# Performance work log

Hardware: AMD Instinct MI355X
Metric: run time of the kernel (lower is better)

Reference implementation:

```python
import jax, jax.numpy as jnp
import numpy as np

B, S, D_IN, D_OUT = 4, 2048, 1024, 1024

def setup_inputs() -> dict:
    key = jax.random.key(0)
    k1, k2, k3, k4 = jax.random.split(key, 4)
    s = 0.02
    return {
        "X": jax.random.normal(k1, (B, S, D_IN), dtype=jnp.float32),
        "Wq": jax.random.normal(k2, (D_OUT, D_IN), dtype=jnp.float32) * s,
        "Wk": jax.random.normal(k3, (D_OUT, D_IN), dtype=jnp.float32) * s,
        "Wv": jax.random.normal(k4, (D_OUT, D_IN), dtype=jnp.float32) * s,
    }

def reference(X, Wq, Wk, Wv):
    # nn.Linear: y = x @ W.T (no bias)
    q = jnp.einsum('bsd,ed->bse', X, Wq)  # [B,S,D_OUT]
    k = jnp.einsum('bsd,ed->bse', X, Wk)
    v = jnp.einsum('bsd,ed->bse', X, Wv)
    scores = jnp.einsum('bqe,bke->bqk', q, k)  # [B,S,S]
    n = X.shape[1]
    causal = jnp.triu(jnp.ones((n, n), dtype=bool), k=1)
    scores = jnp.where(causal[None], -jnp.inf, scores)
    scale = 1.0 / jnp.sqrt(jnp.asarray(k.shape[-1], dtype=scores.dtype))
    attn = jax.nn.softmax(scores * scale, axis=-1)
    return jnp.einsum('bqk,bke->bqe', attn, v)
```

## Files before the change

kernel.cpp:

```cpp
#include <hip/hip_runtime.h>
#include <cstdint>


typedef __attribute__((ext_vector_type(8))) __bf16 bf16x8;
typedef __attribute__((ext_vector_type(4))) float f32x4;

#define BK 64

__device__ __forceinline__ unsigned short f2bf(float f) {
  union { float f; unsigned u; } v; v.f = f;
  unsigned r = v.u + 0x7fffu + ((v.u >> 16) & 1u);
  return (unsigned short)(r >> 16);
}

__device__ __forceinline__ void gload_lds16(const void* g, void* l) {
  __builtin_amdgcn_global_load_lds(
      (const __attribute__((address_space(1))) void*)g,
      (__attribute__((address_space(3))) void*)l, 16, 0, 0);
}

__global__ __launch_bounds__(256)
void cvt_all(const float* __restrict__ X, const float* __restrict__ Wq,
             const float* __restrict__ Wk, const float* __restrict__ Wv,
             unsigned short* __restrict__ Xbf, unsigned short* __restrict__ Wall,
             float* __restrict__ L) {
  const int bid = blockIdx.x;
  if (bid >= 11264) {
    float4* p = (float4*)(L + (size_t)(bid - 11264) * 2048);
    p[threadIdx.x] = (float4){0.f, 0.f, 0.f, 0.f};
    p[threadIdx.x + 256] = (float4){0.f, 0.f, 0.f, 0.f};
    return;
  }
  const float* src;
  unsigned short* dst;
  int i;
  if (bid < 8192) {
    src = X; dst = Xbf; i = bid * 256 + threadIdx.x;
  } else {
    const int m = bid - 8192;
    const int sel = m >> 10;
    src = (sel == 0) ? Wq : (sel == 1) ? Wk : Wv;
    dst = Wall + (size_t)sel * 1048576;
    i = (m & 1023) * 256 + threadIdx.x;
  }
  float4 v = ((const float4*)src)[i];
  ushort4 o;
  o.x = f2bf(v.x); o.y = f2bf(v.y); o.z = f2bf(v.z); o.w = f2bf(v.w);
  ((ushort4*)dst)[i] = o;
}

__global__ __launch_bounds__(256, 3)
void gemm_qkv(const unsigned short* __restrict__ A,
              const unsigned short* __restrict__ Bm,
              unsigned short* __restrict__ Qb,
              unsigned short* __restrict__ Kb,
              unsigned short* __restrict__ Vt)
{
  const int bx = blockIdx.x, by = blockIdx.y;

  __shared__ __align__(16) unsigned short As[128 * BK];
  __shared__ __align__(16) unsigned short Bs[128 * BK];

  const int tid = threadIdx.x;
  const int wave = tid >> 6, lane = tid & 63;
  const int wr = wave >> 1, wc = wave & 1;
  const int quad = lane >> 4, l16 = lane & 15;

  const unsigned rsub = wave * 8 + (lane >> 3);
  const unsigned csb = (unsigned)(((lane & 7) ^ ((lane >> 3) & 7)) * 16);

  unsigned offA[4], offB[4];
  #pragma unroll
  for (int s = 0; s < 4; ++s) {
    offA[s] = ((unsigned)(by * 128 + s * 32 + rsub) * 1024u) * 2u + csb;
    offB[s] = ((unsigned)(bx * 128 + s * 32 + rsub) * 1024u) * 2u + csb;
  }
  const char* Abase = (const char*)A;
  const char* Bbase = (const char*)Bm;

  f32x4 acc[4][4];
  #pragma unroll
  for (int i = 0; i < 4; ++i)
    #pragma unroll
    for (int j = 0; j < 4; ++j)
      acc[i][j] = (f32x4){0.f, 0.f, 0.f, 0.f};

  const int pq = (quad ^ (l16 & 7)) * 8;
  const int aOff = (wr * 64 + l16) * BK + pq;
  const int bOff = (wc * 64 + l16) * BK + pq;

  for (int k0 = 0; k0 < 1024; k0 += BK) {
    const unsigned kb = (unsigned)k0 * 2u;
    #pragma unroll
    for (int s = 0; s < 4; ++s) {
      gload_lds16(Abase + kb + offA[s], As + s * 2048 + wave * 512);
      gload_lds16(Bbase + kb + offB[s], Bs + s * 2048 + wave * 512);
    }
    __syncthreads();
    #pragma unroll
    for (int h = 0; h < 2; ++h) {
      const int hx = h * 32;
      bf16x8 af[4], bfr[4];
      #pragma unroll
      for (int i = 0; i < 4; ++i)
        af[i] = *(const bf16x8*)(As + ((aOff + i * 16 * BK) ^ hx));
      #pragma unroll
      for (int j = 0; j < 4; ++j)
        bfr[j] = *(const bf16x8*)(Bs + ((bOff + j * 16 * BK) ^ hx));
      #pragma unroll
      for (int i = 0; i < 4; ++i)
        #pragma unroll
        for (int j = 0; j < 4; ++j)
          acc[i][j] = __builtin_amdgcn_mfma_f32_16x16x32_bf16(af[i], bfr[j], acc[i][j], 0, 0, 0);
    }
    __syncthreads();
  }

  const int row0 = by * 128 + wr * 64 + quad * 4;
  const int col0 = bx * 128 + wc * 64 + l16;
  if (bx < 16) {
    unsigned short* C = (bx < 8) ? Qb : Kb;
    const int col = (bx < 8) ? col0 : col0 - 1024;
    #pragma unroll
    for (int i = 0; i < 4; ++i)
      #pragma unroll
      for (int r = 0; r < 4; ++r) {
        const size_t rr = (size_t)(row0 + i * 16 + r) * 1024;
        #pragma unroll
        for (int j = 0; j < 4; ++j)
          C[rr + col + j * 16] = f2bf(acc[i][j][r]);
      }
  } else {
    const int b = row0 >> 11;
    const int s0 = row0 & 2047;
    unsigned short* Vb = Vt + (size_t)b * 2097152;
    #pragma unroll
    for (int j = 0; j < 4; ++j) {
      const size_t ee = (size_t)(col0 - 2048 + j * 16) * 2048;
      #pragma unroll
      for (int i = 0; i < 4; ++i) {
        ushort4 o;
        o.x = f2bf(acc[i][j][0]); o.y = f2bf(acc[i][j][1]);
        o.z = f2bf(acc[i][j][2]); o.w = f2bf(acc[i][j][3]);
        *(ushort4*)(Vb + ee + s0 + i * 16) = o;
      }
    }
  }
}

__global__ __launch_bounds__(256, 3)
void gemm_scores(const unsigned short* __restrict__ Q,
                 const unsigned short* __restrict__ Km,
                 unsigned short* __restrict__ S,
                 float* __restrict__ L)
{
  const int t = blockIdx.x;
  const int bz = blockIdx.z;
  int by = (int)((sqrtf(8.f * t + 1.f) - 1.f) * 0.5f);
  while ((by + 1) * (by + 2) / 2 <= t) ++by;
  while (by * (by + 1) / 2 > t) --by;
  const int bx = t - by * (by + 1) / 2;

  __shared__ __align__(16) unsigned short As[128 * BK];
  __shared__ __align__(16) unsigned short Bs[128 * BK];

  const int tid = threadIdx.x;
  const int wave = tid >> 6, lane = tid & 63;
  const int wr = wave >> 1, wc = wave & 1;
  const int quad = lane >> 4, l16 = lane & 15;

  const unsigned rsub = wave * 8 + (lane >> 3);
  const unsigned csb = (unsigned)(((lane & 7) ^ ((lane >> 3) & 7)) * 16);

  unsigned offA[4], offB[4];
  #pragma unroll
  for (int s = 0; s < 4; ++s) {
    offA[s] = ((unsigned)(by * 128 + s * 32 + rsub) * 1024u) * 2u + csb;
    offB[s] = ((unsigned)(bx * 128 + s * 32 + rsub) * 1024u) * 2u + csb;
  }
  const char* Abase = (const char*)(Q + (size_t)bz * 2097152);
  const char* Bbase = (const char*)(Km + (size_t)bz * 2097152);

  f32x4 acc[4][4];
  #pragma unroll
  for (int i = 0; i < 4; ++i)
    #pragma unroll
    for (int j = 0; j < 4; ++j)
      acc[i][j] = (f32x4){0.f, 0.f, 0.f, 0.f};

  const int pq = (quad ^ (l16 & 7)) * 8;
  const int aOff = (wr * 64 + l16) * BK + pq;
  const int bOff = (wc * 64 + l16) * BK + pq;

  for (int k0 = 0; k0 < 1024; k0 += BK) {
    const unsigned kb = (unsigned)k0 * 2u;
    #pragma unroll
    for (int s = 0; s < 4; ++s) {
      gload_lds16(Abase + kb + offA[s], As + s * 2048 + wave * 512);
      gload_lds16(Bbase + kb + offB[s], Bs + s * 2048 + wave * 512);
    }
    __syncthreads();
    #pragma unroll
    for (int h = 0; h < 2; ++h) {
      const int hx = h * 32;
      bf16x8 af[4], bfr[4];
      #pragma unroll
      for (int i = 0; i < 4; ++i)
        af[i] = *(const bf16x8*)(As + ((aOff + i * 16 * BK) ^ hx));
      #pragma unroll
      for (int j = 0; j < 4; ++j)
        bfr[j] = *(const bf16x8*)(Bs + ((bOff + j * 16 * BK) ^ hx));
      #pragma unroll
      for (int i = 0; i < 4; ++i)
        #pragma unroll
        for (int j = 0; j < 4; ++j)
          acc[i][j] = __builtin_amdgcn_mfma_f32_16x16x32_bf16(af[i], bfr[j], acc[i][j], 0, 0, 0);
    }
    __syncthreads();
  }

  const int row0 = by * 128 + wr * 64 + quad * 4;
  const int col0 = bx * 128 + wc * 64 + l16;
  float* Lb = L + (size_t)bz * 2048;
  unsigned short* C = S + (size_t)bz * 4194304;

  #pragma unroll
  for (int i = 0; i < 4; ++i)
    #pragma unroll
    for (int r = 0; r < 4; ++r) {
      const int grow = row0 + i * 16 + r;
      float ps = 0.f;
      #pragma unroll
      for (int j = 0; j < 4; ++j) {
        const int gcol = col0 + j * 16;
        float e = (gcol <= grow) ? __expf(acc[i][j][r] * 0.03125f) : 0.f;
        acc[i][j][r] = e;
        ps += e;
      }
      #pragma unroll
      for (int m = 8; m > 0; m >>= 1)
        ps += __shfl_xor(ps, m);
      if (l16 == 0) atomicAdd(&Lb[grow], ps);
      const size_t rr = (size_t)grow * 2048;
      #pragma unroll
      for (int j = 0; j < 4; ++j)
        C[rr + col0 + j * 16] = f2bf(acc[i][j][r]);
    }
}

__global__ __launch_bounds__(256, 3)
void gemm_pv(const unsigned short* __restrict__ P,
             const unsigned short* __restrict__ Vt,
             float* __restrict__ Out,
             const float* __restrict__ L)
{
  const int bx = blockIdx.x, by = blockIdx.y, bz = blockIdx.z;

  __shared__ __align__(16) unsigned short As[128 * BK];
  __shared__ __align__(16) unsigned short Bs[128 * BK];

  const int tid = threadIdx.x;
  const int wave = tid >> 6, lane = tid & 63;
  const int wr = wave >> 1, wc = wave & 1;
  const int quad = lane >> 4, l16 = lane & 15;

  const unsigned rsub = wave * 8 + (lane >> 3);
  const unsigned csb = (unsigned)(((lane & 7) ^ ((lane >> 3) & 7)) * 16);

  unsigned offA[4], offB[4];
  #pragma unroll
  for (int s = 0; s < 4; ++s) {
    offA[s] = ((unsigned)(by * 128 + s * 32 + rsub) * 2048u) * 2u + csb;
    offB[s] = ((unsigned)(bx * 128 + s * 32 + rsub) * 2048u) * 2u + csb;
  }
  const char* Abase = (const char*)(P + (size_t)bz * 4194304);
  const char* Bbase = (const char*)(Vt + (size_t)bz * 2097152);

  f32x4 acc[4][4];
  #pragma unroll
  for (int i = 0; i < 4; ++i)
    #pragma unroll
    for (int j = 0; j < 4; ++j)
      acc[i][j] = (f32x4){0.f, 0.f, 0.f, 0.f};

  const int kmax = (by + 1) * 128;

  const int pq = (quad ^ (l16 & 7)) * 8;
  const int aOff = (wr * 64 + l16) * BK + pq;
  const int bOff = (wc * 64 + l16) * BK + pq;

  for (int k0 = 0; k0 < kmax; k0 += BK) {
    const unsigned kb = (unsigned)k0 * 2u;
    #pragma unroll
    for (int s = 0; s < 4; ++s) {
      gload_lds16(Abase + kb + offA[s], As + s * 2048 + wave * 512);
      gload_lds16(Bbase + kb + offB[s], Bs + s * 2048 + wave * 512);
    }
    __syncthreads();
    #pragma unroll
    for (int h = 0; h < 2; ++h) {
      const int hx = h * 32;
      bf16x8 af[4], bfr[4];
      #pragma unroll
      for (int i = 0; i < 4; ++i)
        af[i] = *(const bf16x8*)(As + ((aOff + i * 16 * BK) ^ hx));
      #pragma unroll
      for (int j = 0; j < 4; ++j)
        bfr[j] = *(const bf16x8*)(Bs + ((bOff + j * 16 * BK) ^ hx));
      #pragma unroll
      for (int i = 0; i < 4; ++i)
        #pragma unroll
        for (int j = 0; j < 4; ++j)
          acc[i][j] = __builtin_amdgcn_mfma_f32_16x16x32_bf16(af[i], bfr[j], acc[i][j], 0, 0, 0);
    }
    __syncthreads();
  }

  const int row0 = by * 128 + wr * 64 + quad * 4;
  const int col0 = bx * 128 + wc * 64 + l16;
  float* C = Out + (size_t)bz * 2097152;
  const float* Lb = L + (size_t)bz * 2048;
  #pragma unroll
  for (int i = 0; i < 4; ++i)
    #pragma unroll
    for (int r = 0; r < 4; ++r) {
      const int grow = row0 + i * 16 + r;
      const float inv = 1.0f / Lb[grow];
      const size_t rr = (size_t)grow * 1024;
      #pragma unroll
      for (int j = 0; j < 4; ++j)
        C[rr + col0 + j * 16] = acc[i][j][r] * inv;
    }
}

extern "C" void kernel_launch(void* const* d_in, const int* in_sizes, int n_in,
                              void* d_out, int out_size, void* d_ws, size_t ws_size,
                              hipStream_t stream) {
  const float* X  = (const float*)d_in[0];
  const float* Wq = (const float*)d_in[1];
  const float* Wk = (const float*)d_in[2];
  const float* Wv = (const float*)d_in[3];
  float* Out = (float*)d_out;

  char* ws = (char*)d_ws;
  unsigned short* Xbf  = (unsigned short*)(ws);
  unsigned short* Wall = (unsigned short*)(ws + 16777216);
  unsigned short* Qbf  = (unsigned short*)(ws + 23068672);
  unsigned short* Kbf  = (unsigned short*)(ws + 39845888);
  unsigned short* Vt   = (unsigned short*)(ws + 56623104);
  unsigned short* Sbf  = (unsigned short*)(ws + 73400320);
  float*          Lbuf = (float*)(ws + 106954752);

  cvt_all<<<11268, 256, 0, stream>>>(X, Wq, Wk, Wv, Xbf, Wall, Lbuf);

  gemm_qkv<<<dim3(24, 64), 256, 0, stream>>>(Xbf, Wall, Qbf, Kbf, Vt);

  gemm_scores<<<dim3(136, 1, 4), 256, 0, stream>>>(Qbf, Kbf, Sbf, Lbuf);

  gemm_pv<<<dim3(8, 16, 4), 256, 0, stream>>>(Sbf, Vt, Out, Lbuf);
}
```

Before: 227.6 us.

## Rewrite QKV GEMM with 256x256 tiles, double-buffered LDS and phased pipeline

Replaces the 128x128 single-buffered QKV projection GEMM with a 512-thread, 256x256-tile kernel. Global-to-LDS loads are double-buffered and interleaved with MFMA phases, using explicit vmcnt waits, barriers and setprio. A grid swizzle is added for L2 locality. The larger tile improves operand reuse and hides load latency, at the cost of 128KB of LDS, higher register pressure and fragile hand-scheduled synchronization.

```diff
diff --git a/kernel.cpp b/kernel.cpp
--- a/kernel.cpp
+++ b/kernel.cpp
@@ -49,102 +49,166 @@
   ((ushort4*)dst)[i] = o;
 }
 
-__global__ __launch_bounds__(256, 3)
-void gemm_qkv(const unsigned short* __restrict__ A,
-              const unsigned short* __restrict__ Bm,
-              unsigned short* __restrict__ Qb,
-              unsigned short* __restrict__ Kb,
-              unsigned short* __restrict__ Vt)
+
+#define BUFSTR 32768
+#define HSTR   16384
+#define SSTR    8192
+
+#define BAR1 do { asm volatile("s_barrier\n\ts_waitcnt lgkmcnt(0)" ::: "memory"); \
+                  __builtin_amdgcn_sched_barrier(0); } while (0)
+#define BAR2 do { asm volatile("s_barrier" ::: "memory"); } while (0)
+#define VBAR(W) do { asm volatile("s_waitcnt vmcnt(" #W ")\n\ts_barrier" ::: "memory"); } while (0)
+
+#define STG_A(buf, H, s, k2) gload_lds16( \
+    Abase + (offA + (unsigned)(((H)*128 + (s)*64) * 2048) + (k2)), \
+    AsB + ((buf)*BUFSTR + (H)*HSTR + (s)*SSTR) + ldsW)
+#define STG_B(buf, H, s, k2) gload_lds16( \
+    Bbase + (offB + (unsigned)(((H)*128 + (s)*64) * 2048) + (k2)), \
+    BsB + ((buf)*BUFSTR + (H)*HSTR + (s)*SSTR) + ldsW)
+
+#define RD_A(buf, a) do { \
+  const char* _ba = AsB + (buf)*BUFSTR + (a)*HSTR; \
+  _Pragma("unroll") \
+  for (int i = 0; i < 4; ++i) { \
+    af[i][0] = *(const bf16x8*)(_ba + (aRd + (unsigned)i*2048u)); \
+    af[i][1] = *(const bf16x8*)(_ba + ((aRd + (unsigned)i*2048u) ^ 64u)); \
+  } \
+} while (0)
+
+#define RD_B(DST, buf, b) do { \
+  const char* _bb = BsB + (buf)*BUFSTR + (b)*HSTR; \
+  _Pragma("unroll") \
+  for (int j = 0; j < 2; ++j) { \
+    DST[j][0] = *(const bf16x8*)(_bb + (bRd + (unsigned)j*2048u)); \
+    DST[j][1] = *(const bf16x8*)(_bb + ((bRd + (unsigned)j*2048u) ^ 64u)); \
+  } \
+} while (0)
+
+#define MM(aq, bq, BF) do { \
+  __builtin_amdgcn_s_setprio(1); \
+  _Pragma("unroll") \
+  for (int h = 0; h < 2; ++h) \
+    _Pragma("unroll") \
+    for (int i = 0; i < 4; ++i) \
+      _Pragma("unroll") \
+      for (int j = 0; j < 2; ++j) \
+        acc[(aq)*4+i][(bq)*2+j] = __builtin_amdgcn_mfma_f32_16x16x32_bf16( \
+            af[i][h], BF[j][h], acc[(aq)*4+i][(bq)*2+j], 0, 0, 0); \
+  __builtin_amdgcn_s_setprio(0); \
+} while (0)
+
+#define PH1_(p, W)     do { RD_A(p, 0); RD_B(b0, p, 0); BAR1; MM(0,0,b0); VBAR(W); } while (0)
+#define PH2S(p, k2, W) do { RD_B(b1, p, 1); STG_A(p,0,0,k2); STG_A(p,0,1,k2); \
+                            STG_B(p,0,0,k2); STG_B(p,0,1,k2); BAR1; MM(0,1,b1); VBAR(W); } while (0)
+#define PH2N(p, W)     do { RD_B(b1, p, 1); BAR1; MM(0,1,b1); VBAR(W); } while (0)
+#define PH3S(p, k2)    do { RD_A(p, 1); STG_B(p,1,0,k2); STG_B(p,1,1,k2); \
+                            BAR1; MM(1,1,b1); BAR2; } while (0)
+#define PH3N(p)        do { RD_A(p, 1); BAR1; MM(1,1,b1); BAR2; } while (0)
+#define PH4S(p, k2, W) do { STG_A(p,1,0,k2); STG_A(p,1,1,k2); BAR1; MM(1,0,b0); VBAR(W); } while (0)
+#define PH4N(p, W)     do { BAR1; MM(1,0,b0); VBAR(W); } while (0)
+#define PH4E(p)        do { BAR1; MM(1,0,b0); } while (0)
+
+__global__ __launch_bounds__(512, 2)
+void gemm_qkv2(const unsigned short* __restrict__ A,
+               const unsigned short* __restrict__ Bm,
+               unsigned short* __restrict__ Qb,
+               unsigned short* __restrict__ Kb,
+               unsigned short* __restrict__ Vt)
 {
-  const int bx = blockIdx.x, by = blockIdx.y;
-
-  __shared__ __align__(16) unsigned short As[128 * BK];
-  __shared__ __align__(16) unsigned short Bs[128 * BK];
+  const int wg = blockIdx.x;
+  const int swz = (wg & 7) * 48 + (wg >> 3);
+  const int by = swz / 12, bx = swz % 12;
+
+  __shared__ __align__(16) unsigned short As[2][2][128 * 64];
+  __shared__ __align__(16) unsigned short Bs[2][2][128 * 64];
 
   const int tid = threadIdx.x;
   const int wave = tid >> 6, lane = tid & 63;
-  const int wr = wave >> 1, wc = wave & 1;
+  const int wr = wave >> 2, wc = wave & 3;
   const int quad = lane >> 4, l16 = lane & 15;
 
-  const unsigned rsub = wave * 8 + (lane >> 3);
+  const unsigned rsub = (unsigned)(wave * 8 + (lane >> 3));
   const unsigned csb = (unsigned)(((lane & 7) ^ ((lane >> 3) & 7)) * 16);
 
-  unsigned offA[4], offB[4];
-  #pragma unroll
-  for (int s = 0; s < 4; ++s) {
-    offA[s] = ((unsigned)(by * 128 + s * 32 + rsub) * 1024u) * 2u + csb;
-    offB[s] = ((unsigned)(bx * 128 + s * 32 + rsub) * 1024u) * 2u + csb;
-  }
+  const unsigned offA = (unsigned)(by * 256 + rsub) * 2048u + csb;
+  const unsigned offB = (unsigned)(bx * 256 + rsub) * 2048u + csb;
   const char* Abase = (const char*)A;
   const char* Bbase = (const char*)Bm;
-
-  f32x4 acc[4][4];
-  #pragma unroll
-  for (int i = 0; i < 4; ++i)
+  char* AsB = (char*)&As[0][0][0];
+  char* BsB = (char*)&Bs[0][0][0];
+  const unsigned ldsW = (unsigned)(wave * 1024);
+
+  const unsigned aRd = (unsigned)((wr * 64 + l16) * 128) + (unsigned)((quad ^ (l16 & 7)) * 16);
+  const unsigned bRd = (unsigned)((wc * 32 + l16) * 128) + (unsigned)((quad ^ (l16 & 7)) * 16);
+
+  f32x4 acc[8][4];
+  #pragma unroll
+  for (int i = 0; i < 8; ++i)
     #pragma unroll
     for (int j = 0; j < 4; ++j)
       acc[i][j] = (f32x4){0.f, 0.f, 0.f, 0.f};
 
-  const int pq = (quad ^ (l16 & 7)) * 8;
-  const int aOff = (wr * 64 + l16) * BK + pq;
-  const int bOff = (wc * 64 + l16) * BK + pq;
-
-  for (int k0 = 0; k0 < 1024; k0 += BK) {
-    const unsigned kb = (unsigned)k0 * 2u;
-    #pragma unroll
-    for (int s = 0; s < 4; ++s) {
-      gload_lds16(Abase + kb + offA[s], As + s * 2048 + wave * 512);
-      gload_lds16(Bbase + kb + offB[s], Bs + s * 2048 + wave * 512);
-    }
-    __syncthreads();
-    #pragma unroll
-    for (int h = 0; h < 2; ++h) {
-      const int hx = h * 32;
-      bf16x8 af[4], bfr[4];
-      #pragma unroll
-      for (int i = 0; i < 4; ++i)
-        af[i] = *(const bf16x8*)(As + ((aOff + i * 16 * BK) ^ hx));
-      #pragma unroll
-      for (int j = 0; j < 4; ++j)
-        bfr[j] = *(const bf16x8*)(Bs + ((bOff + j * 16 * BK) ^ hx));
+  bf16x8 af[4][2], b0[2][2], b1[2][2];
+
+  STG_A(0,0,0,0u);   STG_A(0,0,1,0u);
+  STG_B(0,0,0,0u);   STG_B(0,0,1,0u);
+  STG_B(0,1,0,0u);   STG_B(0,1,1,0u);
+  STG_A(0,1,0,0u);   STG_A(0,1,1,0u);
+  STG_A(1,0,0,128u); STG_A(1,0,1,128u);
+  STG_B(1,0,0,128u); STG_B(1,0,1,128u);
+  STG_B(1,1,0,128u); STG_B(1,1,1,128u);
+  STG_A(1,1,0,128u); STG_A(1,1,1,128u);
+  VBAR(12);
+
+  #pragma unroll 1
+  for (int it = 0; it < 7; ++it) {
+    const unsigned ka = (unsigned)(2 * it + 2) * 128u;
+    const unsigned kb = (unsigned)(2 * it + 3) * 128u;
+    PH1_(0, 10); PH2S(0, ka, 12); PH3S(0, ka); PH4S(0, ka, 12);
+    PH1_(1, 10); PH2S(1, kb, 12); PH3S(1, kb); PH4S(1, kb, 12);
+  }
+  PH1_(0, 10); PH2N(0, 8); PH3N(0); PH4N(0, 4);
+  PH1_(1, 2);  PH2N(1, 0); PH3N(1); PH4E(1);
+
+  if (bx < 8) {
+    unsigned short* C = (bx < 4) ? Qb : Kb;
+    const int cb = (bx < 4) ? (bx * 256 + wc * 32 + l16)
+                            : (bx * 256 - 1024 + wc * 32 + l16);
+    #pragma unroll
+    for (int aq = 0; aq < 2; ++aq)
       #pragma unroll
       for (int i = 0; i < 4; ++i)
         #pragma unroll
-        for (int j = 0; j < 4; ++j)
-          acc[i][j] = __builtin_amdgcn_mfma_f32_16x16x32_bf16(af[i], bfr[j], acc[i][j], 0, 0, 0);
-    }
-    __syncthreads();
-  }
-
-  const int row0 = by * 128 + wr * 64 + quad * 4;
-  const int col0 = bx * 128 + wc * 64 + l16;
-  if (bx < 16) {
-    unsigned short* C = (bx < 8) ? Qb : Kb;
-    const int col = (bx < 8) ? col0 : col0 - 1024;
-    #pragma unroll
-    for (int i = 0; i < 4; ++i)
-      #pragma unroll
-      for (int r = 0; r < 4; ++r) {
-        const size_t rr = (size_t)(row0 + i * 16 + r) * 1024;
+        for (int r = 0; r < 4; ++r) {
+          const size_t rr = (size_t)(by * 256 + aq * 128 + wr * 64 + i * 16 + quad * 4 + r) * 1024;
+          #pragma unroll
+          for (int bq = 0; bq < 2; ++bq)
+            #pragma unroll
+            for (int j = 0; j < 2; ++j)
+              C[rr + cb + bq * 128 + j * 16] = f2bf(acc[aq * 4 + i][bq * 2 + j][r]);
+        }
+  } else {
+    const int row0 = by * 256 + wr * 64 + quad * 4;
+    const int b = row0 >> 11;
+    unsigned short* Vb = Vt + (size_t)b * 2097152;
+    const int e0 = bx * 256 - 2048 + wc * 32 + l16;
+    #pragma unroll
+    for (int bq = 0; bq < 2; ++bq)
+      #pragma unroll
+      for (int j = 0; j < 2; ++j) {
+        const size_t ee = (size_t)(e0 + bq * 128 + j * 16) * 2048;
         #pragma unroll
-        for (int j = 0; j < 4; ++j)
-          C[rr + col + j * 16] = f2bf(acc[i][j][r]);
+        for (int aq = 0; aq < 2; ++aq)
+          #pragma unroll
+          for (int i = 0; i < 4; ++i) {
+            const int s = (row0 + aq * 128 + i * 16) & 2047;
+            f32x4 a4 = acc[aq * 4 + i][bq * 2 + j];
+            ushort4 o;
+            o.x = f2bf(a4[0]); o.y = f2bf(a4[1]);
+            o.z = f2bf(a4[2]); o.w = f2bf(a4[3]);
+            *(ushort4*)(Vb + ee + s) = o;
+          }
       }
-  } else {
-    const int b = row0 >> 11;
-    const int s0 = row0 & 2047;
-    unsigned short* Vb = Vt + (size_t)b * 2097152;
-    #pragma unroll
-    for (int j = 0; j < 4; ++j) {
-      const size_t ee = (size_t)(col0 - 2048 + j * 16) * 2048;
-      #pragma unroll
-      for (int i = 0; i < 4; ++i) {
-        ushort4 o;
-        o.x = f2bf(acc[i][j][0]); o.y = f2bf(acc[i][j][1]);
-        o.z = f2bf(acc[i][j][2]); o.w = f2bf(acc[i][j][3]);
-        *(ushort4*)(Vb + ee + s0 + i * 16) = o;
-      }
-    }
   }
 }
 
@@ -161,8 +225,8 @@
   while (by * (by + 1) / 2 > t) --by;
   const int bx = t - by * (by + 1) / 2;
 
-  __shared__ __align__(16) unsigned short As[128 * BK];
-  __shared__ __align__(16) unsigned short Bs[128 * BK];
+  __shared__ __align__(16) unsigned short As2[128 * BK];
+  __shared__ __align__(16) unsigned short Bs2[128 * BK];
 
   const int tid = threadIdx.x;
   const int wave = tid >> 6, lane = tid & 63;
@@ -196,8 +260,8 @@
     const unsigned kb = (unsigned)k0 * 2u;
     #pragma unroll
     for (int s = 0; s < 4; ++s) {
-      gload_lds16(Abase + kb + offA[s], As + s * 2048 + wave * 512);
-      gload_lds16(Bbase + kb + offB[s], Bs + s * 2048 + wave * 512);
+      gload_lds16(Abase + kb + offA[s], As2 + s * 2048 + wave * 512);
+      gload_lds16(Bbase + kb + offB[s], Bs2 + s * 2048 + wave * 512);
     }
     __syncthreads();
     #pragma unroll
@@ -206,10 +270,10 @@
       bf16x8 af[4], bfr[4];
       #pragma unroll
       for (int i = 0; i < 4; ++i)
-        af[i] = *(const bf16x8*)(As + ((aOff + i * 16 * BK) ^ hx));
+        af[i] = *(const bf16x8*)(As2 + ((aOff + i * 16 * BK) ^ hx));
       #pragma unroll
       for (int j = 0; j < 4; ++j)
-        bfr[j] = *(const bf16x8*)(Bs + ((bOff + j * 16 * BK) ^ hx));
+        bfr[j] = *(const bf16x8*)(Bs2 + ((bOff + j * 16 * BK) ^ hx));
       #pragma unroll
       for (int i = 0; i < 4; ++i)
         #pragma unroll
@@ -256,8 +320,8 @@
 {
   const int bx = blockIdx.x, by = blockIdx.y, bz = blockIdx.z;
 
-  __shared__ __align__(16) unsigned short As[128 * BK];
-  __shared__ __align__(16) unsigned short Bs[128 * BK];
+  __shared__ __align__(16) unsigned short As2[128 * BK];
+  __shared__ __align__(16) unsigned short Bs2[128 * BK];
 
   const int tid = threadIdx.x;
   const int wave = tid >> 6, lane = tid & 63;
@@ -293,8 +357,8 @@
     const unsigned kb = (unsigned)k0 * 2u;
     #pragma unroll
     for (int s = 0; s < 4; ++s) {
-      gload_lds16(Abase + kb + offA[s], As + s * 2048 + wave * 512);
-      gload_lds16(Bbase + kb + offB[s], Bs + s * 2048 + wave * 512);
+      gload_lds16(Abase + kb + offA[s], As2 + s * 2048 + wave * 512);
+      gload_lds16(Bbase + kb + offB[s], Bs2 + s * 2048 + wave * 512);
     }
     __syncthreads();
     #pragma unroll
@@ -303,10 +367,10 @@
       bf16x8 af[4], bfr[4];
       #pragma unroll
       for (int i = 0; i < 4; ++i)
-        af[i] = *(const bf16x8*)(As + ((aOff + i * 16 * BK) ^ hx));
+        af[i] = *(const bf16x8*)(As2 + ((aOff + i * 16 * BK) ^ hx));
       #pragma unroll
       for (int j = 0; j < 4; ++j)
-        bfr[j] = *(const bf16x8*)(Bs + ((bOff + j * 16 * BK) ^ hx));
+        bfr[j] = *(const bf16x8*)(Bs2 + ((bOff + j * 16 * BK) ^ hx));
       #pragma unroll
       for (int i = 0; i < 4; ++i)
         #pragma unroll
@@ -353,7 +417,7 @@
 
   cvt_all<<<11268, 256, 0, stream>>>(X, Wq, Wk, Wv, Xbf, Wall, Lbuf);
 
-  gemm_qkv<<<dim3(24, 64), 256, 0, stream>>>(Xbf, Wall, Qbf, Kbf, Vt);
+  gemm_qkv2<<<384, 512, 0, stream>>>(Xbf, Wall, Qbf, Kbf, Vt);
 
   gemm_scores<<<dim3(136, 1, 4), 256, 0, stream>>>(Qbf, Kbf, Sbf, Lbuf);
 
```

Result: slower. 233.2 us (+2.4%).
